# Kernel optimization log

Hardware: AMD Instinct MI355X
Metric: run time of the kernel (lower is better)

## Reference

```python
import jax, jax.numpy as jnp
import numpy as np

TAU = 0.07      # temperature from __init__ default
TOP_K = 10      # hardcoded k in torch.topk
DIAG_FILL = -10.0
TOP_SIM_VAL = 0.75


def setup_inputs() -> dict:
    key = jax.random.key(0)
    k1, k2 = jax.random.split(key)
    z1 = jax.random.normal(k1, (4096, 512), dtype=jnp.float32)
    z2 = jax.random.normal(k2, (4096, 512), dtype=jnp.float32)
    return {"z1": z1, "z2": z2}


def reference(z1, z2):
    # AllGather is identity on a single device; grad_scaling=False.
    z = jnp.concatenate([z1, z2], axis=0)                      # [n, d]
    # F.normalize(dim=1): divide by L2 norm (eps-clamped)
    norm = jnp.maximum(jnp.linalg.norm(z, axis=1, keepdims=True), 1e-12)
    z = z / norm
    n = z.shape[0]
    half = n // 2

    # labels: ones at offsets +n/2 and -n/2 == identity rolled by n/2
    labels = jnp.roll(jnp.eye(n, dtype=z.dtype), half, axis=1)  # [n, n]

    sim = z @ z.T                                               # [n, n]

    # top_k_based_on_cos_sim branch: softmax of raw sim (diag still present)
    cos_sim = jax.nn.softmax(sim, axis=1)
    idx = jnp.arange(n)
    # branch mask: 0 on same-half blocks, 1 on cross-half blocks
    mask = ((idx[:, None] < half) ^ (idx[None, :] < half)).astype(z.dtype)
    cos_sim = cos_sim * mask
    _, top_idx = jax.lax.top_k(cos_sim, TOP_K)                  # [n, K]
    top_sim = jnp.zeros((n, n), dtype=z.dtype).at[idx[:, None], top_idx].set(TOP_SIM_VAL)
    labels = jnp.maximum(labels, top_sim)

    # fill diagonal with -10, scale by temperature, row log-softmax
    sim = sim.at[idx, idx].set(DIAG_FILL) / TAU
    logp = jax.nn.log_softmax(sim, axis=1)
    loss = -jnp.sum(logp * labels) / n
    return loss
```

## Files before the change

### kernel.cpp

```cpp
#include <hip/hip_runtime.h>
#include <hip/hip_bf16.h>
#include <stdint.h>

#define N_TOTAL 8192
#define HALF_N  4096
#define DIM     512
#define INV_TAU (1.0f/0.07f)

typedef __attribute__((ext_vector_type(4))) int   i32x4;

#define AS1 __attribute__((address_space(1)))
#define AS3 __attribute__((address_space(3)))

__device__ __forceinline__ uint32_t umax32(uint32_t a, uint32_t b) { return a > b ? a : b; }
__device__ __forceinline__ uint32_t umin32(uint32_t a, uint32_t b) { return a < b ? a : b; }

__device__ __forceinline__ float decode_key(uint32_t key)
{
    ushort h = (key & 0x8000u) ? (ushort)(key ^ 0x8000u) : (ushort)(key ^ 0xFFFFu);
    return (float)(*(_Float16*)&h);
}

__global__ __launch_bounds__(256) void norm_kernel(const float* __restrict__ z1,
                                                   const float* __restrict__ z2,
                                                   char* __restrict__ zq,
                                                   float* __restrict__ inv_qn,
                                                   float* __restrict__ rowsum)
{
    if (threadIdx.x < 4) rowsum[blockIdx.x * 4 + threadIdx.x] = 0.f;

    int row  = blockIdx.x * 4 + (threadIdx.x >> 6);
    int lane = threadIdx.x & 63;
    const float* src = (row < HALF_N) ? (z1 + (size_t)row * DIM)
                                      : (z2 + (size_t)(row - HALF_N) * DIM);
    const float4* p = (const float4*)src;
    float4 a = p[lane * 2];
    float4 b = p[lane * 2 + 1];
    float ss = a.x*a.x + a.y*a.y + a.z*a.z + a.w*a.w
             + b.x*b.x + b.y*b.y + b.z*b.z + b.w*b.w;
#pragma unroll
    for (int o = 1; o < 64; o <<= 1) ss += __shfl_xor(ss, o);
    float sc = 127.0f / fmaxf(sqrtf(ss), 1e-12f);

    float v[8] = {a.x*sc, a.y*sc, a.z*sc, a.w*sc, b.x*sc, b.y*sc, b.z*sc, b.w*sc};
    char c8[8];
    int qq = 0;
#pragma unroll
    for (int j = 0; j < 8; j++) {
        int qi = (int)rintf(v[j]);
        qq += qi * qi;
        c8[j] = (char)qi;
    }
#pragma unroll
    for (int o = 1; o < 64; o <<= 1) qq += __shfl_xor(qq, o);
    if (lane == 0) inv_qn[row] = 1.0f / sqrtf(fmaxf((float)qq, 1.0f));

    *(uint2*)(zq + (size_t)row * DIM + lane * 8) = *(const uint2*)c8;
}

__global__ __launch_bounds__(256, 4) void gemm_kernel(const char* __restrict__ zq,
                                                      const float* __restrict__ inv_qn,
                                                      float* __restrict__ rowsum,
                                                      uint2* __restrict__ partial,
                                                      float* __restrict__ pos_sim)
{
    int orig = blockIdx.x;
    int bid  = (orig & 7) * 260 + (orig >> 3);

    int by = (int)(64.5f - sqrtf(4160.25f - 2.0f * (float)bid));
    int off = 64 * by - (by * (by - 1)) / 2;
    if (off > bid) { --by; off = 64 * by - (by * (by - 1)) / 2; }
    else {
        int offn = 64 * (by + 1) - ((by + 1) * by) / 2;
        if (offn <= bid) { ++by; off = offn; }
    }
    int bx = by + (bid - off);

    const int brow = by * 128;
    const int bcol = bx * 128;

    __shared__ char As[2][128 * 64];
    __shared__ char Bs[2][128 * 64];

    const int t    = threadIdx.x;
    const int w    = t >> 6;
    const int lane = t & 63;
    const int wr   = w >> 1, wc = w & 1;

    i32x4 acc[4][4] = {};

    const int c0 = t, c1 = 256 + t;
    const int r0 = c0 >> 2, r1 = c1 >> 2;
    const int q0 = (c0 & 3) ^ ((r0 >> 1) & 3);
    const int q1 = (c1 & 3) ^ ((r1 >> 1) & 3);
    const size_t gaA0 = (size_t)(brow + r0) * DIM + q0 * 16;
    const size_t gaA1 = (size_t)(brow + r1) * DIM + q1 * 16;
    const size_t gaB0 = (size_t)(bcol + r0) * DIM + q0 * 16;
    const size_t gaB1 = (size_t)(bcol + r1) * DIM + q1 * 16;
    const int l0 = (w * 64) * 16;
    const int l1 = (256 + w * 64) * 16;

#define STAGE(buf, ko) do {                                                        \
    __builtin_amdgcn_global_load_lds((const AS1 uint32_t*)(zq + gaA0 + (ko)),      \
        (AS3 uint32_t*)((char*)As[buf] + l0), 16, 0, 0);                           \
    __builtin_amdgcn_global_load_lds((const AS1 uint32_t*)(zq + gaA1 + (ko)),      \
        (AS3 uint32_t*)((char*)As[buf] + l1), 16, 0, 0);                           \
    __builtin_amdgcn_global_load_lds((const AS1 uint32_t*)(zq + gaB0 + (ko)),      \
        (AS3 uint32_t*)((char*)Bs[buf] + l0), 16, 0, 0);                           \
    __builtin_amdgcn_global_load_lds((const AS1 uint32_t*)(zq + gaB1 + (ko)),      \
        (AS3 uint32_t*)((char*)Bs[buf] + l1), 16, 0, 0);                           \
} while (0)

    STAGE(0, 0);
    __syncthreads();

    int cur = 0;
    for (int kt = 0; kt < DIM / 64; ++kt) {
        if (kt + 1 < DIM / 64) STAGE(cur ^ 1, (kt + 1) * 64);

        i32x4 av[4], bv[4];
#pragma unroll
        for (int m = 0; m < 4; m++) {
            int ro = wr * 64 + m * 16 + (lane & 15);
            int s  = (lane >> 4) ^ ((ro >> 1) & 3);
            av[m] = *(const i32x4*)(As[cur] + ro * 64 + s * 16);
        }
#pragma unroll
        for (int n = 0; n < 4; n++) {
            int ro = wc * 64 + n * 16 + (lane & 15);
            int s  = (lane >> 4) ^ ((ro >> 1) & 3);
            bv[n] = *(const i32x4*)(Bs[cur] + ro * 64 + s * 16);
        }
#pragma unroll
        for (int m = 0; m < 4; m++)
#pragma unroll
            for (int n = 0; n < 4; n++)
                acc[m][n] = __builtin_amdgcn_mfma_i32_16x16x64_i8(av[m], bv[n], acc[m][n], 0, 0, 0);

        __syncthreads();
        cur ^= 1;
    }
#undef STAGE

    const bool is_cross = (brow < HALF_N) && (bcol >= HALF_N);
    const bool off_diag = (bx != by);

    float invc[4];
#pragma unroll
    for (int n = 0; n < 4; n++)
        invc[n] = inv_qn[bcol + wc * 64 + n * 16 + (lane & 15)];

    float    cs[4] = {0.f, 0.f, 0.f, 0.f};
    uint32_t s1[4] = {0u, 0u, 0u, 0u};
    uint32_t s2[4] = {0u, 0u, 0u, 0u};

#pragma unroll
    for (int m = 0; m < 4; m++) {
#pragma unroll
        for (int r = 0; r < 4; r++) {
            int grow = brow + wr * 64 + m * 16 + ((lane >> 4) << 2) + r;
            float invr = inv_qn[grow];
            float rs = 0.f;
            uint32_t t1 = 0u, t2 = 0u;
#pragma unroll
            for (int n = 0; n < 4; n++) {
                int gcol = bcol + wc * 64 + n * 16 + (lane & 15);
                float v  = (float)acc[m][n][r] * (invr * invc[n]);
                float e  = (grow == gcol) ? 0.f : __expf(v * INV_TAU);
                rs += e;
                cs[n] += e;
                if (is_cross) {
                    int cidx = gcol - HALF_N;
                    ushort h;
                    *(_Float16*)&h = (_Float16)v;
                    uint32_t key = ((uint32_t)(ushort)(h ^ (ushort)((ushort)((short)h >> 15) | 0x8000))) << 16;
                    uint32_t xr = key | (uint32_t)(4095 - cidx);
                    uint32_t mn = umin32(t1, xr);
                    t1 = umax32(t1, xr);
                    t2 = umax32(t2, mn);
                    uint32_t xc = key | (uint32_t)(4095 - grow);
                    mn = umin32(s1[n], xc);
                    s1[n] = umax32(s1[n], xc);
                    s2[n] = umax32(s2[n], mn);
                    if (cidx == grow) { pos_sim[grow] = v; pos_sim[gcol] = v; }
                }
            }
            rs += __shfl_xor(rs, 1);
            rs += __shfl_xor(rs, 2);
            rs += __shfl_xor(rs, 4);
            rs += __shfl_xor(rs, 8);
            if ((lane & 15) == 0) atomicAdd(&rowsum[grow], rs);

            if (is_cross) {
#pragma unroll
                for (int o = 1; o < 16; o <<= 1) {
                    uint32_t o1 = __shfl_xor(t1, o);
                    uint32_t o2 = __shfl_xor(t2, o);
                    uint32_t nt2 = umax32(umin32(t1, o1), umax32(t2, o2));
                    t1 = umax32(t1, o1);
                    t2 = nt2;
                }
                if ((lane & 15) == 0)
                    partial[((size_t)grow << 6) + (bx - 32) * 2 + wc] = make_uint2(t1, t2);
            }
        }
    }

    if (off_diag) {
#pragma unroll
        for (int n = 0; n < 4; n++) {
            float c = cs[n];
            c += __shfl_xor(c, 16);
            c += __shfl_xor(c, 32);
            uint32_t a1 = s1[n], a2 = s2[n];
            if (is_cross) {
#pragma unroll
                for (int o = 16; o < 64; o <<= 1) {
                    uint32_t o1 = __shfl_xor(a1, o);
                    uint32_t o2 = __shfl_xor(a2, o);
                    uint32_t nt2 = umax32(umin32(a1, o1), umax32(a2, o2));
                    a1 = umax32(a1, o1);
                    a2 = nt2;
                }
            }
            if (lane < 16) {
                int gcol = bcol + wc * 64 + n * 16 + lane;
                atomicAdd(&rowsum[gcol], c);
                if (is_cross)
                    partial[((size_t)gcol << 6) + by * 2 + wr] = make_uint2(a1, a2);
            }
        }
    }
}

__global__ __launch_bounds__(256) void topk_loss_kernel(const uint2* __restrict__ partial,
                                                        const float* __restrict__ pos_sim,
                                                        const float* __restrict__ rowsum,
                                                        float* __restrict__ contrib)
{
    int i    = blockIdx.x * 4 + (threadIdx.x >> 6);
    int lane = threadIdx.x & 63;

    uint2 p = partial[((size_t)i << 6) + lane];
    uint32_t t1 = p.x, t2 = p.y;

    int posidx = i & (HALF_N - 1);
    float S10 = 0.f; int posflag = 0;
#pragma unroll
    for (int tc = 0; tc < 10; tc++) {
        uint32_t b = umax32(t1, t2);
#pragma unroll
        for (int o = 32; o; o >>= 1)
            b = umax32(b, __shfl_xor(b, o));
        bool w1 = (b == t1);
        bool w2 = (b == t2);
        t1 = w1 ? t2 : t1;
        t2 = (w1 | w2) ? 0u : t2;

        int idx = 4095 - (int)(b & 0xFFFFu);
        S10 += decode_key(b >> 16);
        posflag |= (idx == posidx) ? 1 : 0;
    }

    if (lane == 0) {
        float ps  = pos_sim[i];
        float lse = logf(rowsum[i]);
        float L   = 1.0f + 0.75f * (10 - posflag);
        float sll = INV_TAU * (ps + 0.75f * (S10 - posflag * ps));
        contrib[i] = L * lse - sll;
    }
}

__global__ __launch_bounds__(256) void reduce_kernel(const float* __restrict__ contrib,
                                                     float* __restrict__ out)
{
    int t = threadIdx.x;
    float s = 0.f;
    for (int j = t; j < N_TOTAL; j += 256) s += contrib[j];
#pragma unroll
    for (int o = 1; o < 64; o <<= 1) s += __shfl_xor(s, o);
    __shared__ float wsum[4];
    if ((t & 63) == 0) wsum[t >> 6] = s;
    __syncthreads();
    if (t == 0) out[0] = (wsum[0] + wsum[1] + wsum[2] + wsum[3]) * (1.0f / N_TOTAL);
}

extern "C" void kernel_launch(void* const* d_in, const int* in_sizes, int n_in,
                              void* d_out, int out_size, void* d_ws, size_t ws_size,
                              hipStream_t stream)
{
    const float* z1 = (const float*)d_in[0];
    const float* z2 = (const float*)d_in[1];
    float* out = (float*)d_out;

    char* ws = (char*)d_ws;
    char*   zq      = ws;
    float*  rowsum  = (float*)(ws + 4194304);
    float*  pos_sim = (float*)(ws + 4227072);
    float*  inv_qn  = (float*)(ws + 4259840);
    uint2*  partial = (uint2*)(ws + 4292608);
    float*  contrib = (float*)(ws + 8486912);

    norm_kernel<<<N_TOTAL / 4, 256, 0, stream>>>(z1, z2, zq, inv_qn, rowsum);
    gemm_kernel<<<2080, 256, 0, stream>>>(zq, inv_qn, rowsum, partial, pos_sim);
    topk_loss_kernel<<<N_TOTAL / 4, 256, 0, stream>>>(partial, pos_sim, rowsum, contrib);
    reduce_kernel<<<1, 256, 0, stream>>>(contrib, out);
}
```

Before: 92.04 us.

## Load GEMM operands directly from global memory into registers, dropping LDS staging

The int8 MFMA main loop no longer stages A/B tiles through double-buffered shared memory with global_load_lds and barriers. Each lane now reads its 16-byte fragments straight from global memory, and the K loop is fully unrolled. This removes the LDS traffic and __syncthreads, but gives up tile sharing across the four waves, so global/L2 traffic roughly doubles and load latency is no longer hidden by explicit prefetch.

```diff
diff --git a/kernel.cpp b/kernel.cpp
--- a/kernel.cpp
+++ b/kernel.cpp
@@ -8,9 +8,6 @@
 #define INV_TAU (1.0f/0.07f)
 
 typedef __attribute__((ext_vector_type(4))) int   i32x4;
-
-#define AS1 __attribute__((address_space(1)))
-#define AS3 __attribute__((address_space(3)))
 
 __device__ __forceinline__ uint32_t umax32(uint32_t a, uint32_t b) { return a > b ? a : b; }
 __device__ __forceinline__ uint32_t umin32(uint32_t a, uint32_t b) { return a < b ? a : b; }
@@ -79,9 +76,6 @@
     const int brow = by * 128;
     const int bcol = bx * 128;
 
-    __shared__ char As[2][128 * 64];
-    __shared__ char Bs[2][128 * 64];
-
     const int t    = threadIdx.x;
     const int w    = t >> 6;
     const int lane = t & 63;
@@ -89,58 +83,27 @@
 
     i32x4 acc[4][4] = {};
 
-    const int c0 = t, c1 = 256 + t;
-    const int r0 = c0 >> 2, r1 = c1 >> 2;
-    const int q0 = (c0 & 3) ^ ((r0 >> 1) & 3);
-    const int q1 = (c1 & 3) ^ ((r1 >> 1) & 3);
-    const size_t gaA0 = (size_t)(brow + r0) * DIM + q0 * 16;
-    const size_t gaA1 = (size_t)(brow + r1) * DIM + q1 * 16;
-    const size_t gaB0 = (size_t)(bcol + r0) * DIM + q0 * 16;
-    const size_t gaB1 = (size_t)(bcol + r1) * DIM + q1 * 16;
-    const int l0 = (w * 64) * 16;
-    const int l1 = (256 + w * 64) * 16;
-
-#define STAGE(buf, ko) do {                                                        \
-    __builtin_amdgcn_global_load_lds((const AS1 uint32_t*)(zq + gaA0 + (ko)),      \
-        (AS3 uint32_t*)((char*)As[buf] + l0), 16, 0, 0);                           \
-    __builtin_amdgcn_global_load_lds((const AS1 uint32_t*)(zq + gaA1 + (ko)),      \
-        (AS3 uint32_t*)((char*)As[buf] + l1), 16, 0, 0);                           \
-    __builtin_amdgcn_global_load_lds((const AS1 uint32_t*)(zq + gaB0 + (ko)),      \
-        (AS3 uint32_t*)((char*)Bs[buf] + l0), 16, 0, 0);                           \
-    __builtin_amdgcn_global_load_lds((const AS1 uint32_t*)(zq + gaB1 + (ko)),      \
-        (AS3 uint32_t*)((char*)Bs[buf] + l1), 16, 0, 0);                           \
-} while (0)
-
-    STAGE(0, 0);
-    __syncthreads();
-
-    int cur = 0;
+    const char* pa[4];
+    const char* pb[4];
+#pragma unroll
+    for (int m = 0; m < 4; m++) {
+        pa[m] = zq + (size_t)(brow + wr * 64 + m * 16 + (lane & 15)) * DIM + (lane >> 4) * 16;
+        pb[m] = zq + (size_t)(bcol + wc * 64 + m * 16 + (lane & 15)) * DIM + (lane >> 4) * 16;
+    }
+
+#pragma unroll
     for (int kt = 0; kt < DIM / 64; ++kt) {
-        if (kt + 1 < DIM / 64) STAGE(cur ^ 1, (kt + 1) * 64);
-
         i32x4 av[4], bv[4];
 #pragma unroll
-        for (int m = 0; m < 4; m++) {
-            int ro = wr * 64 + m * 16 + (lane & 15);
-            int s  = (lane >> 4) ^ ((ro >> 1) & 3);
-            av[m] = *(const i32x4*)(As[cur] + ro * 64 + s * 16);
-        }
-#pragma unroll
-        for (int n = 0; n < 4; n++) {
-            int ro = wc * 64 + n * 16 + (lane & 15);
-            int s  = (lane >> 4) ^ ((ro >> 1) & 3);
-            bv[n] = *(const i32x4*)(Bs[cur] + ro * 64 + s * 16);
-        }
+        for (int m = 0; m < 4; m++) av[m] = *(const i32x4*)(pa[m] + kt * 64);
+#pragma unroll
+        for (int n = 0; n < 4; n++) bv[n] = *(const i32x4*)(pb[n] + kt * 64);
 #pragma unroll
         for (int m = 0; m < 4; m++)
 #pragma unroll
             for (int n = 0; n < 4; n++)
                 acc[m][n] = __builtin_amdgcn_mfma_i32_16x16x64_i8(av[m], bv[n], acc[m][n], 0, 0, 0);
-
-        __syncthreads();
-        cur ^= 1;
-    }
-#undef STAGE
+    }
 
     const bool is_cross = (brow < HALF_N) && (bcol >= HALF_N);
     const bool off_diag = (bx != by);
```

Result: slower. 132.9 us (+44.4%).
